# Performance work log

Measured on AMD Instinct MI355X. Metric: run time of the kernel, lower is better.

## Reference

```python
import jax, jax.numpy as jnp
import numpy as np

N_TOKENS = 16384
D_MODEL = 1024
N_SEG = 4
H_SEG = 1024  # intermediate_size (4096) // num_segments


def setup_inputs() -> dict:
    key = jax.random.key(0)
    kx, ki, kg, ku, kd = jax.random.split(key, 5)
    x = jax.random.normal(kx, (N_TOKENS, D_MODEL), dtype=jnp.float32)
    token_segment_indices = jax.random.randint(ki, (N_TOKENS,), 0, N_SEG, dtype=jnp.int64)
    s = 1.0 / np.sqrt(D_MODEL)
    # weights stored [seg, in, out] for x @ W
    gate_w = jax.random.normal(kg, (N_SEG, D_MODEL, H_SEG), dtype=jnp.float32) * s
    up_w = jax.random.normal(ku, (N_SEG, D_MODEL, H_SEG), dtype=jnp.float32) * s
    down_w = jax.random.normal(kd, (N_SEG, H_SEG, D_MODEL), dtype=jnp.float32) * (1.0 / np.sqrt(H_SEG))
    return {
        'x': x,
        'gate_w': gate_w,
        'up_w': up_w,
        'down_w': down_w,
        'token_segment_indices': token_segment_indices,
    }


def reference(x, gate_w, up_w, down_w, token_segment_indices):
    # _forward_with_indices: each token is processed only by its assigned
    # segment's SwiGLU FFN; all other contributions are zero.  We compute each
    # segment densely and mask (jit-friendly, same math as gather->ffn->scatter).
    out = jnp.zeros_like(x)
    for s in range(N_SEG):
        hidden = jax.nn.silu(x @ gate_w[s]) * (x @ up_w[s])  # [N, H_SEG]
        y = hidden @ down_w[s]                                # [N, D_MODEL]
        mask = (token_segment_indices == s)[:, None]
        out = out + jnp.where(mask, y, 0.0)
    return out
```

## Files before the change

### kernel.cpp

```cpp
#include <hip/hip_runtime.h>
#include <hip/hip_bf16.h>
#include <math.h>

#define NT   16384
#define DM   1024
#define NSEG 4
#define BK   64
#define HS   1024

typedef __attribute__((ext_vector_type(8))) short bf16x8;
typedef __attribute__((ext_vector_type(4))) float f32x4;

typedef __attribute__((address_space(1))) unsigned int gu32;
typedef __attribute__((address_space(3))) unsigned int lu32;

__device__ __forceinline__ void gll16(const void* g, void* l) {
  __builtin_amdgcn_global_load_lds((gu32*)(unsigned long long)g,
                                   (lu32*)(unsigned int)(unsigned long long)l,
                                   16, 0, 0);
}

__device__ __forceinline__ unsigned short cvt_bf16(float f) {
  unsigned int u = __float_as_uint(f);
  u += 0x7fffu + ((u >> 16) & 1u);
  return (unsigned short)(u >> 16);
}


__global__ __launch_bounds__(256) void k_scan(const int* __restrict__ idx, int* __restrict__ part) {
  __shared__ int c[9];
  int tid = threadIdx.x;
  if (tid < 9) c[tid] = 0;
  __syncthreads();
  int t = blockIdx.x * 256 + tid;
  int w0 = idx[2 * t], w1 = idx[2 * t + 1];
  int lane = tid & 63;
  unsigned long long m;
#pragma unroll
  for (int q = 0; q < 4; ++q) {
    m = __ballot(w0 == q); if (lane == 0 && m) atomicAdd(&c[q], (int)__popcll(m));
    m = __ballot(w1 == q); if (lane == 0 && m) atomicAdd(&c[4 + q], (int)__popcll(m));
  }
  m = __ballot(w1 != 0);
  if (lane == 0 && m) atomicAdd(&c[8], 1);
  __syncthreads();
  if (tid < 9) part[blockIdx.x * 9 + tid] = c[tid];
}

__global__ void k_base(const int* __restrict__ part, int* __restrict__ meta, int2* __restrict__ table) {
  __shared__ int c[9];
  int t = threadIdx.x;
  if (t < 9) {
    int s = 0;
    for (int b = 0; b < 32; ++b) s += part[b * 9 + t];
    c[t] = s;
  }
  __syncthreads();
  if (t == 0) {
    int flag = (c[8] != 0);
    meta[4] = flag;
    int base = 0;
    for (int s = 0; s < 4; ++s) {
      int cnt = flag ? (c[s] + c[4 + s]) : c[s];
      meta[s] = cnt; meta[5 + s] = base; meta[9 + s] = base;
      base += cnt;
    }
    int nt = 0;
    for (int s = 0; s < 4; ++s)
      for (int m0 = 0; m0 < meta[s]; m0 += 128) table[nt++] = make_int2(s, m0);
    for (; nt < 132; ++nt) table[nt] = make_int2(-1, 0);
  }
}

__global__ void k_rank(const int* __restrict__ idx, int* __restrict__ meta,
                       int* __restrict__ rank, int* __restrict__ perm) {
  int t = blockIdx.x * 256 + threadIdx.x;
  int s = meta[4] ? idx[t] : idx[2 * t];
  int lane = threadIdx.x & 63;
  unsigned long long lt = (1ull << lane) - 1;
#pragma unroll
  for (int q = 0; q < 4; ++q) {
    unsigned long long m = __ballot(s == q);
    int wb = 0;
    if (lane == 0 && m) wb = atomicAdd(&meta[9 + q], (int)__popcll(m));
    wb = __shfl(wb, 0);
    if (s == q) {
      int r = wb + (int)__popcll(m & lt);
      rank[t] = r;
      perm[r] = t;
    }
  }
}

__global__ __launch_bounds__(256) void k_prep(
    const float4* __restrict__ x, const int* __restrict__ rank, uint4* __restrict__ xc,
    const float* __restrict__ gw, const float* __restrict__ uw,
    unsigned short* __restrict__ gwt, unsigned short* __restrict__ uwt) {
  __shared__ float tile[64][65];
  int bid = blockIdx.x, tid = threadIdx.x;
  if (bid < 8192) {
    int tok = bid * 2 + (tid >> 7);
    int li = tid & 127;
    int r = rank[tok];
    float4 a = x[tok * 256 + li * 2];
    float4 b = x[tok * 256 + li * 2 + 1];
    uint4 o;
    o.x = cvt_bf16(a.x) | ((unsigned)cvt_bf16(a.y) << 16);
    o.y = cvt_bf16(a.z) | ((unsigned)cvt_bf16(a.w) << 16);
    o.z = cvt_bf16(b.x) | ((unsigned)cvt_bf16(b.y) << 16);
    o.w = cvt_bf16(b.z) | ((unsigned)cvt_bf16(b.w) << 16);
    xc[r * 128 + li] = o;
    return;
  }
  int tb = bid - 8192;
  int mtx = tb >> 10, seg = (tb >> 8) & 3, tl = tb & 255;
  const float* src = (mtx == 0 ? gw : uw) + (size_t)seg * DM * HS;
  unsigned short* dst = (mtx == 0 ? gwt : uwt) + (size_t)seg * DM * HS;
  int n0 = (tl & 15) * 64, k0 = (tl >> 4) * 64;
  int col = tid & 63, rb = tid >> 6;
#pragma unroll
  for (int i = 0; i < 64; i += 4)
    tile[i + rb][col] = src[(size_t)(k0 + i + rb) * 1024 + n0 + col];
  __syncthreads();
  int kp = tid & 31, nb = tid >> 5;
#pragma unroll
  for (int j = 0; j < 64; j += 8) {
    int nn = j + nb;
    unsigned int w = (unsigned)cvt_bf16(tile[2 * kp][nn]) |
                     ((unsigned)cvt_bf16(tile[2 * kp + 1][nn]) << 16);
    *(unsigned int*)(dst + (size_t)(n0 + nn) * 1024 + k0 + 2 * kp) = w;
  }
}

__global__ __launch_bounds__(256) void k_gateup(
    const unsigned short* __restrict__ xc,
    const unsigned short* __restrict__ gwt,
    const unsigned short* __restrict__ uwt,
    const int* __restrict__ meta,
    const int2* __restrict__ table,
    const float* __restrict__ dw,
    unsigned short* __restrict__ dwt,
    unsigned short* __restrict__ hidden) {
  union Sm {
    struct { unsigned short As[128 * BK], Bg[64 * BK], Bu[64 * BK]; } g;
    float tile[64][65];
  };
  __shared__ Sm sm;
  const int bid = blockIdx.x, tid = threadIdx.x;

  if (bid < 1024) {
    int seg = bid >> 8, tl = bid & 255;
    int n0t = (tl & 15) * 64, k0t = (tl >> 4) * 64;
    const float* src = dw + (size_t)seg * DM * HS;
    unsigned short* dst = dwt + (size_t)seg * DM * HS;
    int col = tid & 63, rb = tid >> 6;
#pragma unroll
    for (int i = 0; i < 64; i += 4)
      sm.tile[i + rb][col] = src[(size_t)(k0t + i + rb) * 1024 + n0t + col];
    __syncthreads();
    int kp = tid & 31, nb = tid >> 5;
#pragma unroll
    for (int j = 0; j < 64; j += 8) {
      int nn = j + nb;
      unsigned int w = (unsigned)cvt_bf16(sm.tile[2 * kp][nn]) |
                       ((unsigned)cvt_bf16(sm.tile[2 * kp + 1][nn]) << 16);
      *(unsigned int*)(dst + (size_t)(n0t + nn) * 1024 + k0t + 2 * kp) = w;
    }
    return;
  }

  const int g = bid - 1024;
  const int2 te = table[g >> 4];
  if (te.x < 0) return;
  const int seg = te.x, m0 = te.y;
  const int count = meta[seg], base = meta[5 + seg];
  const int n0 = (g & 15) * 64;

  const int lane = tid & 63;
  const int wave = tid >> 6;

  const unsigned short* ap[4];
#pragma unroll
  for (int is = 0; is < 4; ++is) {
    int c = is * 256 + tid;
    int m = c >> 3;
    int kb = (c & 7) ^ (m & 7);
    int row = m0 + m;
    row = row < count ? row : count - 1;
    ap[is] = xc + (size_t)(base + row) * DM + kb * 8;
  }
  const unsigned short *gp[2], *up[2];
#pragma unroll
  for (int is = 0; is < 2; ++is) {
    int c = is * 256 + tid;
    int n = c >> 3;
    int kb = (c & 7) ^ (n & 7);
    gp[is] = gwt + (size_t)(seg * HS + n0 + n) * DM + kb * 8;
    up[is] = uwt + (size_t)(seg * HS + n0 + n) * DM + kb * 8;
  }

  f32x4 accg[4][2] = {};
  f32x4 accu[4][2] = {};
  const int wm = (wave & 1) * 64;
  const int wn = (wave >> 1) * 32;
  const int fm = lane & 15;
  const int fq = lane >> 4;
  const int fx = lane & 7;
  const int a_e0 = (wm + fm) * 64 + ((fq) ^ fx) * 8;
  const int a_e1 = (wm + fm) * 64 + ((4 + fq) ^ fx) * 8;
  const int b_e0 = (wn + fm) * 64 + ((fq) ^ fx) * 8;
  const int b_e1 = (wn + fm) * 64 + ((4 + fq) ^ fx) * 8;

  for (int kt = 0; kt < DM / BK; ++kt) {
    __syncthreads();
#pragma unroll
    for (int is = 0; is < 4; ++is)
      gll16(ap[is], (char*)sm.g.As + (is * 256 + wave * 64) * 16);
#pragma unroll
    for (int is = 0; is < 2; ++is) {
      gll16(gp[is], (char*)sm.g.Bg + (is * 256 + wave * 64) * 16);
      gll16(up[is], (char*)sm.g.Bu + (is * 256 + wave * 64) * 16);
    }
#pragma unroll
    for (int is = 0; is < 4; ++is) ap[is] += BK;
#pragma unroll
    for (int is = 0; is < 2; ++is) { gp[is] += BK; up[is] += BK; }
    __syncthreads();
#pragma unroll
    for (int s = 0; s < 2; ++s) {
      const unsigned short* Ap = sm.g.As + (s ? a_e1 : a_e0);
      const unsigned short* Gp = sm.g.Bg + (s ? b_e1 : b_e0);
      const unsigned short* Up = sm.g.Bu + (s ? b_e1 : b_e0);
      bf16x8 af[4], bg2[2], bu2[2];
#pragma unroll
      for (int mi = 0; mi < 4; ++mi) af[mi] = *(const bf16x8*)(Ap + mi * 1024);
#pragma unroll
      for (int ni = 0; ni < 2; ++ni) {
        bg2[ni] = *(const bf16x8*)(Gp + ni * 1024);
        bu2[ni] = *(const bf16x8*)(Up + ni * 1024);
      }
#pragma unroll
      for (int mi = 0; mi < 4; ++mi)
#pragma unroll
        for (int ni = 0; ni < 2; ++ni) {
          accg[mi][ni] = __builtin_amdgcn_mfma_f32_16x16x32_bf16(af[mi], bg2[ni], accg[mi][ni], 0, 0, 0);
          accu[mi][ni] = __builtin_amdgcn_mfma_f32_16x16x32_bf16(af[mi], bu2[ni], accu[mi][ni], 0, 0, 0);
        }
    }
  }

  const int rq = fq * 4;
#pragma unroll
  for (int mi = 0; mi < 4; ++mi) {
#pragma unroll
    for (int r = 0; r < 4; ++r) {
      int row = m0 + wm + mi * 16 + rq + r;
      if (row < count) {
        unsigned short* h = hidden + (size_t)(base + row) * HS + n0 + wn;
#pragma unroll
        for (int ni = 0; ni < 2; ++ni) {
          float gv = accg[mi][ni][r];
          float uv = accu[mi][ni][r];
          float sig = 1.0f / (1.0f + __expf(-gv));
          h[ni * 16 + fm] = cvt_bf16(gv * sig * uv);
        }
      }
    }
  }
}

__global__ __launch_bounds__(256) void k_down(
    const unsigned short* __restrict__ hidden,
    const unsigned short* __restrict__ dwt,
    const int* __restrict__ meta,
    const int2* __restrict__ table,
    const int* __restrict__ perm,
    float* __restrict__ out) {
  __shared__ __align__(16) unsigned short As[128 * BK];
  __shared__ __align__(16) unsigned short Bs[128 * BK];
  const int bid = blockIdx.x, tid = threadIdx.x;
  const int2 te = table[bid >> 3];
  if (te.x < 0) return;
  const int seg = te.x, m0 = te.y;
  const int count = meta[seg], base = meta[5 + seg];
  const int n0 = (bid & 7) * 128;

  const int lane = tid & 63;
  const int wave = tid >> 6;

  const unsigned short *ap[4], *bp[4];
#pragma unroll
  for (int is = 0; is < 4; ++is) {
    int c = is * 256 + tid;
    int m = c >> 3;
    int kb = (c & 7) ^ (m & 7);
    int row = m0 + m;
    row = row < count ? row : count - 1;
    ap[is] = hidden + (size_t)(base + row) * HS + kb * 8;
    bp[is] = dwt + (size_t)(seg * DM + n0 + m) * HS + kb * 8;
  }

  f32x4 acc[4][4] = {};
  const int wm = (wave & 1) * 64;
  const int wn = (wave >> 1) * 64;
  const int fm = lane & 15;
  const int fq = lane >> 4;
  const int fx = lane & 7;
  const int a_e0 = (wm + fm) * 64 + ((fq) ^ fx) * 8;
  const int a_e1 = (wm + fm) * 64 + ((4 + fq) ^ fx) * 8;
  const int b_e0 = (wn + fm) * 64 + ((fq) ^ fx) * 8;
  const int b_e1 = (wn + fm) * 64 + ((4 + fq) ^ fx) * 8;

  for (int kt = 0; kt < HS / BK; ++kt) {
    __syncthreads();
#pragma unroll
    for (int is = 0; is < 4; ++is) {
      gll16(ap[is], (char*)As + (is * 256 + wave * 64) * 16);
      gll16(bp[is], (char*)Bs + (is * 256 + wave * 64) * 16);
    }
#pragma unroll
    for (int is = 0; is < 4; ++is) { ap[is] += BK; bp[is] += BK; }
    __syncthreads();
#pragma unroll
    for (int s = 0; s < 2; ++s) {
      const unsigned short* Ap = As + (s ? a_e1 : a_e0);
      const unsigned short* Bp = Bs + (s ? b_e1 : b_e0);
      bf16x8 af[4], bf[4];
#pragma unroll
      for (int mi = 0; mi < 4; ++mi) af[mi] = *(const bf16x8*)(Ap + mi * 1024);
#pragma unroll
      for (int ni = 0; ni < 4; ++ni) bf[ni] = *(const bf16x8*)(Bp + ni * 1024);
#pragma unroll
      for (int mi = 0; mi < 4; ++mi)
#pragma unroll
        for (int ni = 0; ni < 4; ++ni)
          acc[mi][ni] = __builtin_amdgcn_mfma_f32_16x16x32_bf16(af[mi], bf[ni], acc[mi][ni], 0, 0, 0);
    }
  }

  const int rq = fq * 4;
#pragma unroll
  for (int mi = 0; mi < 4; ++mi) {
#pragma unroll
    for (int r = 0; r < 4; ++r) {
      int row = m0 + wm + mi * 16 + rq + r;
      if (row < count) {
        int t = perm[base + row];
        float* o = out + (size_t)t * DM + n0 + wn;
#pragma unroll
        for (int ni = 0; ni < 4; ++ni)
          o[ni * 16 + fm] = acc[mi][ni][r];
      }
    }
  }
}


extern "C" void kernel_launch(void* const* d_in, const int* in_sizes, int n_in,
                              void* d_out, int out_size, void* d_ws, size_t ws_size,
                              hipStream_t stream) {
  const float* x  = (const float*)d_in[0];
  const float* gw = (const float*)d_in[1];
  const float* uw = (const float*)d_in[2];
  const float* dw = (const float*)d_in[3];
  const int* tsi  = (const int*)d_in[4];
  float* out = (float*)d_out;

  char* ws = (char*)d_ws;
  int* meta  = (int*)ws;
  int* part  = (int*)(ws + 256);
  int2* table = (int2*)(ws + 2048);
  int* rank  = (int*)(ws + 4096);
  int* perm  = (int*)(ws + 4096 + NT * 4);
  unsigned short* xc  = (unsigned short*)(ws + (1 << 18));
  unsigned short* gwt = xc + (size_t)NT * DM;
  unsigned short* uwt = gwt + (size_t)NSEG * HS * DM;
  unsigned short* dwt = uwt + (size_t)NSEG * HS * DM;
  unsigned short* hid = dwt + (size_t)NSEG * DM * HS;

  k_scan<<<32, 256, 0, stream>>>(tsi, part);
  k_base<<<1, 64, 0, stream>>>(part, meta, table);
  k_rank<<<NT / 256, 256, 0, stream>>>(tsi, meta, rank, perm);
  k_prep<<<8192 + 2048, 256, 0, stream>>>((const float4*)x, rank, (uint4*)xc, gw, uw, gwt, uwt);
  k_gateup<<<1024 + 16 * 132, 256, 0, stream>>>(xc, gwt, uwt, meta, table, dw, dwt, hid);
  k_down<<<8 * 132, 256, 0, stream>>>(hid, dwt, meta, table, perm, out);
}
```

Measured before the change: 334.2 us.

## Fuse routing scan/rank into fewer kernels and move down-weight transpose to prep

```diff
diff --git a/kernel.cpp b/kernel.cpp
--- a/kernel.cpp
+++ b/kernel.cpp
@@ -27,108 +27,129 @@
 }
 
 
-__global__ __launch_bounds__(256) void k_scan(const int* __restrict__ idx, int* __restrict__ part) {
-  __shared__ int c[9];
-  int tid = threadIdx.x;
-  if (tid < 9) c[tid] = 0;
-  __syncthreads();
-  int t = blockIdx.x * 256 + tid;
-  int w0 = idx[2 * t], w1 = idx[2 * t + 1];
-  int lane = tid & 63;
-  unsigned long long m;
+__global__ __launch_bounds__(256) void k_prepw(
+    const int* __restrict__ idx, int* __restrict__ part,
+    const float* __restrict__ gw, const float* __restrict__ uw, const float* __restrict__ dw,
+    unsigned short* __restrict__ gwt, unsigned short* __restrict__ uwt,
+    unsigned short* __restrict__ dwt) {
+  __shared__ float tile[64][65];
+  const int bid = blockIdx.x, tid = threadIdx.x;
+  if (bid < 64) {
+    __shared__ int sc[5];
+    if (tid < 5) sc[tid] = 0;
+    __syncthreads();
+    int lane = tid & 63;
+    int w32 = idx[bid * 256 + tid];
+    unsigned long long m = __ballot((tid & 1) && (w32 != 0));
+    if (lane == 0 && m) atomicAdd(&sc[4], 1);
+    __syncthreads();
+    int is32 = (sc[4] != 0);
+    int s = w32;
+    if (!is32) s = idx[bid * 512 + 2 * tid];
+#pragma unroll
+    for (int q = 0; q < 4; ++q) {
+      m = __ballot(s == q);
+      if (lane == 0 && m) atomicAdd(&sc[q], (int)__popcll(m));
+    }
+    __syncthreads();
+    if (tid < 4) part[bid * 8 + tid] = sc[tid];
+    if (tid == 4) part[bid * 8 + 4] = is32;
+    return;
+  }
+  int tb = bid - 64;
+  int mtx = tb >> 10, seg = (tb >> 8) & 3, tl = tb & 255;
+  const float* src = (mtx == 0 ? gw : mtx == 1 ? uw : dw) + (size_t)seg * DM * HS;
+  unsigned short* dst = (mtx == 0 ? gwt : mtx == 1 ? uwt : dwt) + (size_t)seg * DM * HS;
+  int n0 = (tl & 15) * 64, k0 = (tl >> 4) * 64;
+  int col = tid & 63, rb = tid >> 6;
+#pragma unroll
+  for (int i = 0; i < 64; i += 4)
+    tile[i + rb][col] = src[(size_t)(k0 + i + rb) * 1024 + n0 + col];
+  __syncthreads();
+  int kp = tid & 31, nb = tid >> 5;
+#pragma unroll
+  for (int j = 0; j < 64; j += 8) {
+    int nn = j + nb;
+    unsigned int w = (unsigned)cvt_bf16(tile[2 * kp][nn]) |
+                     ((unsigned)cvt_bf16(tile[2 * kp + 1][nn]) << 16);
+    *(unsigned int*)(dst + (size_t)(n0 + nn) * 1024 + k0 + 2 * kp) = w;
+  }
+}
+
+__global__ __launch_bounds__(256) void k_cvtrank(
+    const int* __restrict__ idx, const int* __restrict__ part,
+    const float4* __restrict__ x,
+    int* __restrict__ meta, int2* __restrict__ table,
+    int* __restrict__ perm, uint4* __restrict__ xc) {
+  __shared__ int cnt[64][4];
+  __shared__ int wsum[4][4];
+  __shared__ int tot[4], pref[4], gbase[4];
+  __shared__ int rnk8[8];
+  __shared__ int flag_s;
+  const int tid = threadIdx.x, bid = blockIdx.x;
+  const int lane = tid & 63, wv = tid >> 6;
+  const int c = bid >> 5;
+  const int p0 = (bid & 31) * 8;
+
+  if (tid == 0) flag_s = part[c * 8 + 4];
+  if (wv == 0) {
+#pragma unroll
+    for (int s = 0; s < 4; ++s) cnt[lane][s] = part[lane * 8 + s];
+  }
+  __syncthreads();
+  const int is32 = flag_s;
+  int tok = c * 256 + tid;
+  int s_t = is32 ? idx[tok] : idx[2 * tok];
+  int myr = 0;
+  unsigned long long lt = (1ull << lane) - 1;
 #pragma unroll
   for (int q = 0; q < 4; ++q) {
-    m = __ballot(w0 == q); if (lane == 0 && m) atomicAdd(&c[q], (int)__popcll(m));
-    m = __ballot(w1 == q); if (lane == 0 && m) atomicAdd(&c[4 + q], (int)__popcll(m));
-  }
-  m = __ballot(w1 != 0);
-  if (lane == 0 && m) atomicAdd(&c[8], 1);
-  __syncthreads();
-  if (tid < 9) part[blockIdx.x * 9 + tid] = c[tid];
-}
-
-__global__ void k_base(const int* __restrict__ part, int* __restrict__ meta, int2* __restrict__ table) {
-  __shared__ int c[9];
-  int t = threadIdx.x;
-  if (t < 9) {
-    int s = 0;
-    for (int b = 0; b < 32; ++b) s += part[b * 9 + t];
-    c[t] = s;
-  }
-  __syncthreads();
-  if (t == 0) {
-    int flag = (c[8] != 0);
-    meta[4] = flag;
-    int base = 0;
-    for (int s = 0; s < 4; ++s) {
-      int cnt = flag ? (c[s] + c[4 + s]) : c[s];
-      meta[s] = cnt; meta[5 + s] = base; meta[9 + s] = base;
-      base += cnt;
-    }
-    int nt = 0;
-    for (int s = 0; s < 4; ++s)
-      for (int m0 = 0; m0 < meta[s]; m0 += 128) table[nt++] = make_int2(s, m0);
-    for (; nt < 132; ++nt) table[nt] = make_int2(-1, 0);
-  }
-}
-
-__global__ void k_rank(const int* __restrict__ idx, int* __restrict__ meta,
-                       int* __restrict__ rank, int* __restrict__ perm) {
-  int t = blockIdx.x * 256 + threadIdx.x;
-  int s = meta[4] ? idx[t] : idx[2 * t];
-  int lane = threadIdx.x & 63;
-  unsigned long long lt = (1ull << lane) - 1;
-#pragma unroll
-  for (int q = 0; q < 4; ++q) {
-    unsigned long long m = __ballot(s == q);
-    int wb = 0;
-    if (lane == 0 && m) wb = atomicAdd(&meta[9 + q], (int)__popcll(m));
-    wb = __shfl(wb, 0);
-    if (s == q) {
-      int r = wb + (int)__popcll(m & lt);
-      rank[t] = r;
-      perm[r] = t;
-    }
-  }
-}
-
-__global__ __launch_bounds__(256) void k_prep(
-    const float4* __restrict__ x, const int* __restrict__ rank, uint4* __restrict__ xc,
-    const float* __restrict__ gw, const float* __restrict__ uw,
-    unsigned short* __restrict__ gwt, unsigned short* __restrict__ uwt) {
-  __shared__ float tile[64][65];
-  int bid = blockIdx.x, tid = threadIdx.x;
-  if (bid < 8192) {
-    int tok = bid * 2 + (tid >> 7);
-    int li = tid & 127;
-    int r = rank[tok];
-    float4 a = x[tok * 256 + li * 2];
-    float4 b = x[tok * 256 + li * 2 + 1];
+    unsigned long long m = __ballot(s_t == q);
+    if (lane == 0) wsum[wv][q] = (int)__popcll(m);
+    if (s_t == q) myr = (int)__popcll(m & lt);
+  }
+  __syncthreads();
+  if (tid < 4) {
+    int s = tid, t = 0, p = 0;
+    for (int b = 0; b < 64; ++b) { if (b == c) p = t; t += cnt[b][s]; }
+    tot[s] = t; pref[s] = p;
+  }
+  __syncthreads();
+  if (tid == 0) {
+    gbase[0] = 0;
+    for (int s = 1; s < 4; ++s) gbase[s] = gbase[s - 1] + tot[s - 1];
+    if (bid == 0) {
+      int nt = 0;
+      for (int s = 0; s < 4; ++s) {
+        meta[s] = tot[s]; meta[5 + s] = gbase[s];
+        for (int m0 = 0; m0 < tot[s]; m0 += 128) table[nt++] = make_int2(s, m0);
+      }
+      for (; nt < 132; ++nt) table[nt] = make_int2(-1, 0);
+    }
+  }
+  __syncthreads();
+  int wpre = 0;
+  for (int w2 = 0; w2 < wv; ++w2) wpre += wsum[w2][s_t];
+  int r = gbase[s_t] + pref[s_t] + wpre + myr;
+  if (tid >= p0 && tid < p0 + 8) {
+    perm[r] = tok;
+    rnk8[tid - p0] = r;
+  }
+  __syncthreads();
+  const int j = tid >> 5, l2 = tid & 31;
+  const int tok8 = bid * 8 + j;
+  const float4* src = x + (size_t)tok8 * 256;
+  uint4* dst = xc + (size_t)rnk8[j] * 128;
+#pragma unroll
+  for (int it = 0; it < 4; ++it) {
+    float4 a = src[it * 64 + l2 * 2];
+    float4 b = src[it * 64 + l2 * 2 + 1];
     uint4 o;
     o.x = cvt_bf16(a.x) | ((unsigned)cvt_bf16(a.y) << 16);
     o.y = cvt_bf16(a.z) | ((unsigned)cvt_bf16(a.w) << 16);
     o.z = cvt_bf16(b.x) | ((unsigned)cvt_bf16(b.y) << 16);
     o.w = cvt_bf16(b.z) | ((unsigned)cvt_bf16(b.w) << 16);
-    xc[r * 128 + li] = o;
-    return;
-  }
-  int tb = bid - 8192;
-  int mtx = tb >> 10, seg = (tb >> 8) & 3, tl = tb & 255;
-  const float* src = (mtx == 0 ? gw : uw) + (size_t)seg * DM * HS;
-  unsigned short* dst = (mtx == 0 ? gwt : uwt) + (size_t)seg * DM * HS;
-  int n0 = (tl & 15) * 64, k0 = (tl >> 4) * 64;
-  int col = tid & 63, rb = tid >> 6;
-#pragma unroll
-  for (int i = 0; i < 64; i += 4)
-    tile[i + rb][col] = src[(size_t)(k0 + i + rb) * 1024 + n0 + col];
-  __syncthreads();
-  int kp = tid & 31, nb = tid >> 5;
-#pragma unroll
-  for (int j = 0; j < 64; j += 8) {
-    int nn = j + nb;
-    unsigned int w = (unsigned)cvt_bf16(tile[2 * kp][nn]) |
-                     ((unsigned)cvt_bf16(tile[2 * kp + 1][nn]) << 16);
-    *(unsigned int*)(dst + (size_t)(n0 + nn) * 1024 + k0 + 2 * kp) = w;
+    dst[it * 32 + l2] = o;
   }
 }
 
@@ -138,43 +159,16 @@
     const unsigned short* __restrict__ uwt,
     const int* __restrict__ meta,
     const int2* __restrict__ table,
-    const float* __restrict__ dw,
-    unsigned short* __restrict__ dwt,
     unsigned short* __restrict__ hidden) {
-  union Sm {
-    struct { unsigned short As[128 * BK], Bg[64 * BK], Bu[64 * BK]; } g;
-    float tile[64][65];
-  };
-  __shared__ Sm sm;
+  __shared__ __align__(16) unsigned short As[128 * BK];
+  __shared__ __align__(16) unsigned short Bg[64 * BK];
+  __shared__ __align__(16) unsigned short Bu[64 * BK];
   const int bid = blockIdx.x, tid = threadIdx.x;
-
-  if (bid < 1024) {
-    int seg = bid >> 8, tl = bid & 255;
-    int n0t = (tl & 15) * 64, k0t = (tl >> 4) * 64;
-    const float* src = dw + (size_t)seg * DM * HS;
-    unsigned short* dst = dwt + (size_t)seg * DM * HS;
-    int col = tid & 63, rb = tid >> 6;
-#pragma unroll
-    for (int i = 0; i < 64; i += 4)
-      sm.tile[i + rb][col] = src[(size_t)(k0t + i + rb) * 1024 + n0t + col];
-    __syncthreads();
-    int kp = tid & 31, nb = tid >> 5;
-#pragma unroll
-    for (int j = 0; j < 64; j += 8) {
-      int nn = j + nb;
-      unsigned int w = (unsigned)cvt_bf16(sm.tile[2 * kp][nn]) |
-                       ((unsigned)cvt_bf16(sm.tile[2 * kp + 1][nn]) << 16);
-      *(unsigned int*)(dst + (size_t)(n0t + nn) * 1024 + k0t + 2 * kp) = w;
-    }
-    return;
-  }
-
-  const int g = bid - 1024;
-  const int2 te = table[g >> 4];
+  const int2 te = table[bid >> 4];
   if (te.x < 0) return;
   const int seg = te.x, m0 = te.y;
   const int count = meta[seg], base = meta[5 + seg];
-  const int n0 = (g & 15) * 64;
+  const int n0 = (bid & 15) * 64;
 
   const int lane = tid & 63;
   const int wave = tid >> 6;
@@ -215,11 +209,11 @@
     __syncthreads();
 #pragma unroll
     for (int is = 0; is < 4; ++is)
-      gll16(ap[is], (char*)sm.g.As + (is * 256 + wave * 64) * 16);
+      gll16(ap[is], (char*)As + (is * 256 + wave * 64) * 16);
 #pragma unroll
     for (int is = 0; is < 2; ++is) {
-      gll16(gp[is], (char*)sm.g.Bg + (is * 256 + wave * 64) * 16);
-      gll16(up[is], (char*)sm.g.Bu + (is * 256 + wave * 64) * 16);
+      gll16(gp[is], (char*)Bg + (is * 256 + wave * 64) * 16);
+      gll16(up[is], (char*)Bu + (is * 256 + wave * 64) * 16);
     }
 #pragma unroll
     for (int is = 0; is < 4; ++is) ap[is] += BK;
@@ -228,9 +222,9 @@
     __syncthreads();
 #pragma unroll
     for (int s = 0; s < 2; ++s) {
-      const unsigned short* Ap = sm.g.As + (s ? a_e1 : a_e0);
-      const unsigned short* Gp = sm.g.Bg + (s ? b_e1 : b_e0);
-      const unsigned short* Up = sm.g.Bu + (s ? b_e1 : b_e0);
+      const unsigned short* Ap = As + (s ? a_e1 : a_e0);
+      const unsigned short* Gp = Bg + (s ? b_e1 : b_e0);
+      const unsigned short* Up = Bu + (s ? b_e1 : b_e0);
       bf16x8 af[4], bg2[2], bu2[2];
 #pragma unroll
       for (int mi = 0; mi < 4; ++mi) af[mi] = *(const bf16x8*)(Ap + mi * 1024);
@@ -367,21 +361,18 @@
   float* out = (float*)d_out;
 
   char* ws = (char*)d_ws;
-  int* meta  = (int*)ws;
-  int* part  = (int*)(ws + 256);
-  int2* table = (int2*)(ws + 2048);
-  int* rank  = (int*)(ws + 4096);
-  int* perm  = (int*)(ws + 4096 + NT * 4);
+  int*  meta  = (int*)ws;
+  int*  part  = (int*)(ws + 256);
+  int2* table = (int2*)(ws + 4096);
+  int*  perm  = (int*)(ws + 8192);
   unsigned short* xc  = (unsigned short*)(ws + (1 << 18));
   unsigned short* gwt = xc + (size_t)NT * DM;
   unsigned short* uwt = gwt + (size_t)NSEG * HS * DM;
   unsigned short* dwt = uwt + (size_t)NSEG * HS * DM;
   unsigned short* hid = dwt + (size_t)NSEG * DM * HS;
 
-  k_scan<<<32, 256, 0, stream>>>(tsi, part);
-  k_base<<<1, 64, 0, stream>>>(part, meta, table);
-  k_rank<<<NT / 256, 256, 0, stream>>>(tsi, meta, rank, perm);
-  k_prep<<<8192 + 2048, 256, 0, stream>>>((const float4*)x, rank, (uint4*)xc, gw, uw, gwt, uwt);
-  k_gateup<<<1024 + 16 * 132, 256, 0, stream>>>(xc, gwt, uwt, meta, table, dw, dwt, hid);
+  k_prepw<<<64 + 3072, 256, 0, stream>>>(tsi, part, gw, uw, dw, gwt, uwt, dwt);
+  k_cvtrank<<<2048, 256, 0, stream>>>(tsi, part, (const float4*)x, meta, table, perm, (uint4*)xc);
+  k_gateup<<<16 * 132, 256, 0, stream>>>(xc, gwt, uwt, meta, table, hid);
   k_down<<<8 * 132, 256, 0, stream>>>(hid, dwt, meta, table, perm, out);
 }
```

Measured after the change: 321.2 us. 3.9% less time.
